# Kernel tuning notes

Hardware: AMD Instinct MI355X
Metric: run time of the kernel (lower is better)

The kernel has to match this reference:

```python
import jax, jax.numpy as jnp
import numpy as np

RADIUS = 0.05      # outer ball-query radius
MIN_RADIUS = 0.02  # inner exclusion radius


def setup_inputs() -> dict:
    key = jax.random.key(0)
    k1, k2 = jax.random.split(key)
    # raw layout is [B, C, N, 1] as consumed by forward's squeeze(-1).permute(0,2,1)
    xyz = jax.random.uniform(k1, (4, 3, 4096, 1), dtype=jnp.float32)      # coords in unit cube
    points = jax.random.normal(k2, (4, 64, 4096, 1), dtype=jnp.float32)   # per-point features
    return {"xyz": xyz, "points": points}


def _pairwise_sqdist(x):
    # x: [B, N, 3] -> [B, N, N] squared euclidean distances
    sq = jnp.sum(x * x, axis=-1)  # [B, N]
    return sq[:, :, None] + sq[:, None, :] - 2.0 * jnp.einsum('bnc,bmc->bnm', x, x)


def reference(xyz, points):
    # [B, C, N, 1] -> [B, N, C]
    _xyz = jnp.transpose(xyz[..., 0], (0, 2, 1))       # [B, N, 3]
    _points = jnp.transpose(points[..., 0], (0, 2, 1))  # [B, N, D]
    B, N, C = _xyz.shape

    # downsample_query_ball: ball-query neighbor counts in annulus (min_radius, radius),
    # keep the N//2 densest points
    d2 = _pairwise_sqdist(_xyz)                              # [B, N, N]
    nbr_cnt = jnp.sum(((d2 < RADIUS ** 2) & (d2 > MIN_RADIUS ** 2)).astype(jnp.int32), axis=-1)
    _, idx = jax.lax.top_k(nbr_cnt, N // 2)                  # [B, N//2]

    # index_points: gather along the point axis
    new_xyz = jnp.take_along_axis(_xyz, idx[..., None], axis=1)        # [B, N//2, 3]
    new_points = jnp.take_along_axis(_points, idx[..., None], axis=1)  # [B, N//2, D]
    return new_xyz, new_points
```

## Files before the change

kernel.cpp:

```cpp
#include <hip/hip_runtime.h>


#define BN 4
#define NPTS 4096
#define ND 64
#define KSEL 2048
#define R2 0.0025f
#define M2 0.0004f

#define IPT 4
#define ITILES 4
#define JC 32
#define JCH 128

__global__ __launch_bounds__(256) void count_part_kernel(
        const float* __restrict__ xyz, int* __restrict__ part) {
    __shared__ float4 sj[JCH];
    const int jc = blockIdx.x & (JC - 1);
    const int it = (blockIdx.x >> 5) & (ITILES - 1);
    const int b  = blockIdx.x >> 7;
    const float* base = xyz + (size_t)b * 3 * NPTS;

    if (threadIdx.x < JCH) {
        int j = jc * JCH + threadIdx.x;
        float x = base[j], y = base[NPTS + j], z = base[2 * NPTS + j];
        float sq = __fadd_rn(__fadd_rn(__fmul_rn(x, x), __fmul_rn(y, y)),
                             __fmul_rn(z, z));
        sj[threadIdx.x] = make_float4(x, y, z, sq);
    }
    const int ibase = it * 1024 + threadIdx.x;
    float4 mi[IPT];
    #pragma unroll
    for (int k = 0; k < IPT; ++k) {
        int i = ibase + k * 256;
        float x = base[i], y = base[NPTS + i], z = base[2 * NPTS + i];
        float sq = __fadd_rn(__fadd_rn(__fmul_rn(x, x), __fmul_rn(y, y)),
                             __fmul_rn(z, z));
        mi[k] = make_float4(x, y, z, sq);
    }
    __syncthreads();

    int cnt[IPT] = {0, 0, 0, 0};
    #pragma unroll 4
    for (int j = 0; j < JCH; ++j) {
        float4 p = sj[j];
        #pragma unroll
        for (int k = 0; k < IPT; ++k) {
            float dot = __fadd_rn(__fadd_rn(__fmul_rn(mi[k].x, p.x),
                                            __fmul_rn(mi[k].y, p.y)),
                                  __fmul_rn(mi[k].z, p.z));
            float d2 = __fsub_rn(__fadd_rn(mi[k].w, p.w), __fmul_rn(2.0f, dot));
            cnt[k] += (d2 < R2 && d2 > M2) ? 1 : 0;
        }
    }
    int* pp = part + (size_t)((b * ITILES + it) * JC + jc) * 1024;
    #pragma unroll
    for (int k = 0; k < IPT; ++k) pp[threadIdx.x + k * 256] = cnt[k];
}

__global__ __launch_bounds__(256) void rank_gather_kernel(
        const float* __restrict__ xyz, const float* __restrict__ points,
        const int* __restrict__ part, float* __restrict__ out) {
    __shared__ alignas(16) int skey[NPTS];
    __shared__ int spr[4][64];
    __shared__ int srank[64];
    const int b     = blockIdx.x >> 6;
    const int tbase = (blockIdx.x & 63) * 64;
    const int tid   = threadIdx.x;

    {
        int4* sk4 = (int4*)skey;
        const int* pbase = part + (size_t)b * ITILES * JC * 1024;
        #pragma unroll
        for (int gg = 0; gg < 4; ++gg) {
            const int g    = tid + gg * 256;
            const int it   = g >> 8;
            const int loc4 = (g & 255) * 4;
            const int4* pp =
                (const int4*)(pbase + (size_t)it * JC * 1024 + loc4);
            int4 s = make_int4(0, 0, 0, 0);
            #pragma unroll 8
            for (int jc = 0; jc < JC; ++jc) {
                int4 v = pp[jc * 256];
                s.x += v.x; s.y += v.y; s.z += v.z; s.w += v.w;
            }
            const int i0 = it * 1024 + loc4;
            int4 kv;
            kv.x = (s.x << 12) | (NPTS - 1 - (i0 + 0));
            kv.y = (s.y << 12) | (NPTS - 1 - (i0 + 1));
            kv.z = (s.z << 12) | (NPTS - 1 - (i0 + 2));
            kv.w = (s.w << 12) | (NPTS - 1 - (i0 + 3));
            sk4[g] = kv;
        }
    }
    __syncthreads();

    {
        const int pi = tid & 63;
        const int q  = tid >> 6;
        const int ki = skey[tbase + pi];
        const int4* sk4 = (const int4*)skey;
        int r = 0;
        #pragma unroll 8
        for (int jj = q * 256; jj < q * 256 + 256; ++jj) {
            int4 v = sk4[jj];
            r += (v.x > ki) ? 1 : 0;
            r += (v.y > ki) ? 1 : 0;
            r += (v.z > ki) ? 1 : 0;
            r += (v.w > ki) ? 1 : 0;
        }
        spr[q][pi] = r;
    }
    __syncthreads();

    if (tid < 64) {
        const int rank = spr[0][tid] + spr[1][tid] + spr[2][tid] + spr[3][tid];
        srank[tid] = rank;
        const int i = tbase + tid;
        if (rank < KSEL) {
            const float* xb = xyz + (size_t)b * 3 * NPTS;
            float* o = out + ((size_t)b * KSEL + rank) * 3;
            o[0] = xb[i]; o[1] = xb[NPTS + i]; o[2] = xb[2 * NPTS + i];
        }
    }
    __syncthreads();

    {
        const int ii   = tid & 63;
        const int q    = tid >> 6;
        const int rank = srank[ii];
        float* ofeat = out + (size_t)BN * KSEL * 3;
        #pragma unroll
        for (int r16 = 0; r16 < 16; ++r16) {
            const int c = q + 4 * r16;
            float v = points[((size_t)b * ND + c) * NPTS + tbase + ii];
            if (rank < KSEL) ofeat[((size_t)b * KSEL + rank) * ND + c] = v;
        }
    }
}

extern "C" void kernel_launch(void* const* d_in, const int* in_sizes, int n_in,
                              void* d_out, int out_size, void* d_ws, size_t ws_size,
                              hipStream_t stream) {
    const float* xyz    = (const float*)d_in[0];
    const float* points = (const float*)d_in[1];
    float* out = (float*)d_out;
    int* part = (int*)d_ws;

    count_part_kernel<<<BN * ITILES * JC, 256, 0, stream>>>(xyz, part);
    rank_gather_kernel<<<BN * 64, 256, 0, stream>>>(xyz, points, part, out);
}
```

Before: 90.38 us.

## Pack distance math into float2 vectors and store partial counts as uint16

The count kernel now processes pairs of j-points with 2-wide float vectors so the compiler can emit packed FP32 ops, with the shared-memory tile split into two SoA-ish float4 arrays. Partial neighbor counts are written as 16-bit values, halving workspace traffic, and the rank kernel sums them packed two per 32-bit lane. Packed summation relies on each half staying below 65536, which holds since a point's count is at most 4096. FP contraction is disabled so the rounding still matches the reference.

```diff
diff --git a/kernel.cpp b/kernel.cpp
--- a/kernel.cpp
+++ b/kernel.cpp
@@ -1,5 +1,7 @@
 #include <hip/hip_runtime.h>
 
+
+#pragma clang fp contract(off)
 
 #define BN 4
 #define NPTS 4096
@@ -12,55 +14,73 @@
 #define ITILES 4
 #define JC 32
 #define JCH 128
+#define JP (JCH / 2)
+
+typedef float f32x2 __attribute__((ext_vector_type(2)));
 
 __global__ __launch_bounds__(256) void count_part_kernel(
-        const float* __restrict__ xyz, int* __restrict__ part) {
-    __shared__ float4 sj[JCH];
+        const float* __restrict__ xyz, unsigned short* __restrict__ part) {
+    __shared__ float4 sA[JP];
+    __shared__ float4 sB[JP];
     const int jc = blockIdx.x & (JC - 1);
     const int it = (blockIdx.x >> 5) & (ITILES - 1);
     const int b  = blockIdx.x >> 7;
     const float* base = xyz + (size_t)b * 3 * NPTS;
 
-    if (threadIdx.x < JCH) {
-        int j = jc * JCH + threadIdx.x;
-        float x = base[j], y = base[NPTS + j], z = base[2 * NPTS + j];
-        float sq = __fadd_rn(__fadd_rn(__fmul_rn(x, x), __fmul_rn(y, y)),
-                             __fmul_rn(z, z));
-        sj[threadIdx.x] = make_float4(x, y, z, sq);
+    if (threadIdx.x < JP) {
+        int j0 = jc * JCH + 2 * threadIdx.x;
+        float2 xv = *(const float2*)(base + j0);
+        float2 yv = *(const float2*)(base + NPTS + j0);
+        float2 zv = *(const float2*)(base + 2 * NPTS + j0);
+        float sq0 = __fadd_rn(__fadd_rn(__fmul_rn(xv.x, xv.x),
+                                        __fmul_rn(yv.x, yv.x)),
+                              __fmul_rn(zv.x, zv.x));
+        float sq1 = __fadd_rn(__fadd_rn(__fmul_rn(xv.y, xv.y),
+                                        __fmul_rn(yv.y, yv.y)),
+                              __fmul_rn(zv.y, zv.y));
+        sA[threadIdx.x] = make_float4(xv.x, xv.y, yv.x, yv.y);
+        sB[threadIdx.x] = make_float4(zv.x, zv.y, sq0, sq1);
     }
     const int ibase = it * 1024 + threadIdx.x;
-    float4 mi[IPT];
+    f32x2 mx[IPT], my[IPT], mz[IPT], ms[IPT];
     #pragma unroll
     for (int k = 0; k < IPT; ++k) {
         int i = ibase + k * 256;
         float x = base[i], y = base[NPTS + i], z = base[2 * NPTS + i];
         float sq = __fadd_rn(__fadd_rn(__fmul_rn(x, x), __fmul_rn(y, y)),
                              __fmul_rn(z, z));
-        mi[k] = make_float4(x, y, z, sq);
+        mx[k] = (f32x2){x, x};  my[k] = (f32x2){y, y};
+        mz[k] = (f32x2){z, z};  ms[k] = (f32x2){sq, sq};
     }
     __syncthreads();
 
     int cnt[IPT] = {0, 0, 0, 0};
-    #pragma unroll 4
-    for (int j = 0; j < JCH; ++j) {
-        float4 p = sj[j];
+    const f32x2 two2 = {2.0f, 2.0f};
+    #pragma unroll 2
+    for (int jp = 0; jp < JP; ++jp) {
+        float4 A = sA[jp], B = sB[jp];
+        f32x2 px = {A.x, A.y}, py = {A.z, A.w};
+        f32x2 pz = {B.x, B.y}, pw = {B.z, B.w};
         #pragma unroll
         for (int k = 0; k < IPT; ++k) {
-            float dot = __fadd_rn(__fadd_rn(__fmul_rn(mi[k].x, p.x),
-                                            __fmul_rn(mi[k].y, p.y)),
-                                  __fmul_rn(mi[k].z, p.z));
-            float d2 = __fsub_rn(__fadd_rn(mi[k].w, p.w), __fmul_rn(2.0f, dot));
-            cnt[k] += (d2 < R2 && d2 > M2) ? 1 : 0;
+            f32x2 t0  = mx[k] * px;
+            f32x2 t1  = my[k] * py;
+            f32x2 t2  = mz[k] * pz;
+            f32x2 dot = (t0 + t1) + t2;
+            f32x2 d2  = (ms[k] + pw) - two2 * dot;
+            cnt[k] += (d2.x < R2 && d2.x > M2) ? 1 : 0;
+            cnt[k] += (d2.y < R2 && d2.y > M2) ? 1 : 0;
         }
     }
-    int* pp = part + (size_t)((b * ITILES + it) * JC + jc) * 1024;
+    unsigned short* pp = part + (size_t)((b * ITILES + it) * JC + jc) * 1024;
     #pragma unroll
-    for (int k = 0; k < IPT; ++k) pp[threadIdx.x + k * 256] = cnt[k];
+    for (int k = 0; k < IPT; ++k)
+        pp[threadIdx.x + k * 256] = (unsigned short)cnt[k];
 }
 
 __global__ __launch_bounds__(256) void rank_gather_kernel(
         const float* __restrict__ xyz, const float* __restrict__ points,
-        const int* __restrict__ part, float* __restrict__ out) {
+        const unsigned short* __restrict__ part, float* __restrict__ out) {
     __shared__ alignas(16) int skey[NPTS];
     __shared__ int spr[4][64];
     __shared__ int srank[64];
@@ -69,28 +89,32 @@
     const int tid   = threadIdx.x;
 
     {
-        int4* sk4 = (int4*)skey;
-        const int* pbase = part + (size_t)b * ITILES * JC * 1024;
+        const unsigned short* pbase = part + (size_t)b * ITILES * JC * 1024;
         #pragma unroll
-        for (int gg = 0; gg < 4; ++gg) {
+        for (int gg = 0; gg < 2; ++gg) {
             const int g    = tid + gg * 256;
-            const int it   = g >> 8;
-            const int loc4 = (g & 255) * 4;
+            const int it   = g >> 7;
+            const int loc8 = (g & 127) * 8;
             const int4* pp =
-                (const int4*)(pbase + (size_t)it * JC * 1024 + loc4);
+                (const int4*)(pbase + (size_t)it * JC * 1024 + loc8);
             int4 s = make_int4(0, 0, 0, 0);
             #pragma unroll 8
             for (int jc = 0; jc < JC; ++jc) {
-                int4 v = pp[jc * 256];
+                int4 v = pp[jc * 128];
                 s.x += v.x; s.y += v.y; s.z += v.z; s.w += v.w;
             }
-            const int i0 = it * 1024 + loc4;
-            int4 kv;
-            kv.x = (s.x << 12) | (NPTS - 1 - (i0 + 0));
-            kv.y = (s.y << 12) | (NPTS - 1 - (i0 + 1));
-            kv.z = (s.z << 12) | (NPTS - 1 - (i0 + 2));
-            kv.w = (s.w << 12) | (NPTS - 1 - (i0 + 3));
-            sk4[g] = kv;
+            const int i0 = it * 1024 + loc8;
+            int4 ka, kb;
+            ka.x = ((s.x & 0xFFFF) << 12)          | (NPTS - 1 - (i0 + 0));
+            ka.y = (((unsigned)s.x >> 16) << 12)   | (NPTS - 1 - (i0 + 1));
+            ka.z = ((s.y & 0xFFFF) << 12)          | (NPTS - 1 - (i0 + 2));
+            ka.w = (((unsigned)s.y >> 16) << 12)   | (NPTS - 1 - (i0 + 3));
+            kb.x = ((s.z & 0xFFFF) << 12)          | (NPTS - 1 - (i0 + 4));
+            kb.y = (((unsigned)s.z >> 16) << 12)   | (NPTS - 1 - (i0 + 5));
+            kb.z = ((s.w & 0xFFFF) << 12)          | (NPTS - 1 - (i0 + 6));
+            kb.w = (((unsigned)s.w >> 16) << 12)   | (NPTS - 1 - (i0 + 7));
+            ((int4*)skey)[g * 2]     = ka;
+            ((int4*)skey)[g * 2 + 1] = kb;
         }
     }
     __syncthreads();
@@ -145,7 +169,7 @@
     const float* xyz    = (const float*)d_in[0];
     const float* points = (const float*)d_in[1];
     float* out = (float*)d_out;
-    int* part = (int*)d_ws;
+    unsigned short* part = (unsigned short*)d_ws;
 
     count_part_kernel<<<BN * ITILES * JC, 256, 0, stream>>>(xyz, part);
     rank_gather_kernel<<<BN * 64, 256, 0, stream>>>(xyz, points, part, out);
```

New measurement: 89.41 us. About the same (-1.1%).
